# Kernel tuning notes

Measured on AMD Instinct MI355X. Metric: run time of the kernel, lower is better.

The kernel has to match this reference:

```python
import jax, jax.numpy as jnp
import numpy as np
from jax import lax

EMB = 30
K = 5

def leaky(x):
    return jnp.where(x > 0, x, 0.1 * x)

def conv_resid(x, W, b):
    # x: [L, EMB]; W: [EMB, EMB, 3]; SAME trigram conv (matches torch pad=2 + slice) + residual
    y = lax.conv_general_dilated(x.T[None], W, window_strides=(1,), padding=[(1, 1)])  # [1,EMB,L]
    y = leaky(y + b[None, :, None])
    return y[0].T + x

def cosine_sim(A, B):
    num = A @ B.T                                   # [Qa, Qb]
    den = jnp.linalg.norm(A, axis=1)[:, None] * jnp.linalg.norm(B, axis=1)[None, :]
    return num / den

def kmax_pool(sim):
    top = lax.top_k(sim, K)[0]                      # [Q, K] descending
    return jnp.stack([top[:, 0], top.mean(axis=-1)], axis=-1)  # [Q, 2]

def get_output(pools, w, W1, W2):
    temp = jnp.concatenate(pools, axis=-1)          # [Q, 6]
    lo = leaky(temp @ W1.T) @ W2.T                  # [Q, 1]
    lo = lo[:, 0] * w
    return lo.sum() / lo.shape[0]

def setup_inputs() -> dict:
    key = jax.random.key(0)
    ks = jax.random.split(key, 12)
    Q, D = 2048, 8192
    inp = {
        "doc1_embeds": jax.random.normal(ks[0], (D, EMB), jnp.float32),
        "doc2_embeds": jax.random.normal(ks[1], (D, EMB), jnp.float32),
        "question_embeds": jax.random.normal(ks[2], (Q, EMB), jnp.float32),
        "q_idfs": jax.random.uniform(ks[3], (Q, 1), jnp.float32),
        "gaf": jax.random.uniform(ks[4], (4,), jnp.float32),
        "baf": jax.random.uniform(ks[5], (4,), jnp.float32),
        "W_conv": jax.random.normal(ks[6], (EMB, EMB, 3), jnp.float32) * 0.1,
        "b_conv": jax.random.normal(ks[7], (EMB,), jnp.float32) * 0.1,
        "W_qw": jax.random.normal(ks[8], (1, EMB + 1), jnp.float32) * 0.1,
        "W_q1": jax.random.normal(ks[9], (8, 6), jnp.float32) * 0.3,
        "W_q2": jax.random.normal(ks[10], (1, 8), jnp.float32) * 0.3,
        "W_out": jax.random.normal(ks[11], (1, 5), jnp.float32) * 0.3,
    }
    return inp

def reference(doc1_embeds, doc2_embeds, question_embeds, q_idfs, gaf, baf,
              W_conv, b_conv, W_qw, W_q1, W_q2, W_out):
    sim_i_d1 = cosine_sim(question_embeds, doc1_embeds)
    sim_i_d2 = cosine_sim(question_embeds, doc2_embeds)
    sim_oh_d1 = (sim_i_d1 > 1 - 0.001).astype(jnp.float32)
    sim_oh_d2 = (sim_i_d2 > 1 - 0.001).astype(jnp.float32)
    q_conv = conv_resid(question_embeds, W_conv, b_conv)
    d1_conv = conv_resid(doc1_embeds, W_conv, b_conv)
    d2_conv = conv_resid(doc2_embeds, W_conv, b_conv)
    sim_s_d1 = cosine_sim(q_conv, d1_conv)
    sim_s_d2 = cosine_sim(q_conv, d2_conv)
    q_weights = jax.nn.softmax((jnp.concatenate([q_conv, q_idfs], axis=-1) @ W_qw.T)[:, 0])
    doc1_emit = get_output([kmax_pool(sim_oh_d1), kmax_pool(sim_i_d1), kmax_pool(sim_s_d1)], q_weights, W_q1, W_q2)
    doc2_emit = get_output([kmax_pool(sim_oh_d2), kmax_pool(sim_i_d2), kmax_pool(sim_s_d2)], q_weights, W_q1, W_q2)
    good_out = jnp.concatenate([gaf, doc1_emit[None]]) @ W_out.T  # [1]
    bad_out = jnp.concatenate([baf, doc2_emit[None]]) @ W_out.T   # [1]
    loss1 = jnp.sum(jax.nn.relu(1.0 + bad_out - good_out), axis=-1)
    return (loss1, good_out, bad_out)
```

## Files before the change

### kernel.cpp

```cpp
#include <hip/hip_runtime.h>
#include <hip/hip_bf16.h>
#include <math.h>

#define EMB 30
#define NS 64
#define JT 128
#define SUB 64

typedef __attribute__((ext_vector_type(8))) short bf16x8;
typedef __attribute__((ext_vector_type(4))) float f32x4;
typedef __attribute__((ext_vector_type(4))) unsigned u32x4;
typedef __attribute__((ext_vector_type(2))) _Float16 f16x2;

__device__ __forceinline__ float leakyf(float x) { return x > 0.0f ? x : 0.1f * x; }

__device__ __forceinline__ unsigned short f2b(float x) {
  __hip_bfloat16 h = __float2bfloat16(x);
  union { __hip_bfloat16 h; unsigned short u; } cv;
  cv.h = h;
  return cv.u;
}

__device__ __forceinline__ unsigned pkmax(unsigned a, unsigned b) {
  unsigned d;
  asm("v_pk_max_f16 %0, %1, %2" : "=v"(d) : "v"(a), "v"(b));
  return d;
}
__device__ __forceinline__ unsigned pkmin(unsigned a, unsigned b) {
  unsigned d;
  asm("v_pk_min_f16 %0, %1, %2" : "=v"(d) : "v"(a), "v"(b));
  return d;
}
__device__ __forceinline__ unsigned cvtpku(float a, float b) {
  return __builtin_bit_cast(unsigned, __builtin_amdgcn_cvt_pkrtz(a, b));
}

__device__ __forceinline__ void ins5h(unsigned (&t)[5], unsigned v) {
  unsigned n0 = pkmax(t[0], v);
  unsigned n1 = pkmax(pkmin(t[0], v), t[1]);
  unsigned n2 = pkmax(pkmin(t[1], v), t[2]);
  unsigned n3 = pkmax(pkmin(t[2], v), t[3]);
  unsigned n4 = pkmax(pkmin(t[3], v), t[4]);
  t[0] = n0; t[1] = n1; t[2] = n2; t[3] = n3; t[4] = n4;
}

__device__ __forceinline__ void merge5h(unsigned (&a)[5], const unsigned (&b)[5]) {
  unsigned c0 = pkmax(a[0], b[0]);
  unsigned c1 = pkmax(pkmax(pkmin(a[0], b[0]), a[1]), b[1]);
  unsigned c2 = pkmax(pkmax(pkmin(a[0], b[1]), pkmin(a[1], b[0])), pkmax(a[2], b[2]));
  unsigned c3 = pkmax(pkmax(pkmin(a[0], b[2]), pkmin(a[1], b[1])),
                      pkmax(pkmin(a[2], b[0]), pkmax(a[3], b[3])));
  unsigned c4 = pkmax(pkmax(pkmax(pkmin(a[0], b[3]), pkmin(a[1], b[2])),
                            pkmax(pkmin(a[2], b[1]), pkmin(a[3], b[0]))),
                      pkmax(a[4], b[4]));
  a[0] = c0; a[1] = c1; a[2] = c2; a[3] = c3; a[4] = c4;
}

__device__ __forceinline__ void merge5(float (&a)[5], const float (&b)[5]) {
  float c0 = fmaxf(a[0], b[0]);
  float c1 = fmaxf(fmaxf(fminf(a[0], b[0]), a[1]), b[1]);
  float c2 = fmaxf(fmaxf(fminf(a[0], b[1]), fminf(a[1], b[0])), fmaxf(a[2], b[2]));
  float c3 = fmaxf(fmaxf(fminf(a[0], b[2]), fminf(a[1], b[1])),
                   fmaxf(fminf(a[2], b[0]), fmaxf(a[3], b[3])));
  float c4 = fmaxf(fmaxf(fmaxf(fminf(a[0], b[3]), fminf(a[1], b[2])),
                         fmaxf(fminf(a[2], b[1]), fminf(a[3], b[0]))),
                   fmaxf(a[4], b[4]));
  a[0] = c0; a[1] = c1; a[2] = c2; a[3] = c3; a[4] = c4;
}

__global__ __launch_bounds__(256) void prep_all_kernel(
    const float* __restrict__ Xq, const float* __restrict__ X1,
    const float* __restrict__ X2, int Q, int D,
    const float* __restrict__ Wc, const float* __restrict__ bc,
    const float* __restrict__ qidf, const float* __restrict__ Wqw,
    unsigned short* __restrict__ qr, unsigned short* __restrict__ qc,
    unsigned short* __restrict__ cmb, float* __restrict__ logits) {
  __shared__ float sX[66 * EMB];
  __shared__ float sW[EMB * EMB * 3];
  __shared__ float sB[EMB];
  __shared__ float sQw[EMB + 1];
  int tid = threadIdx.x;
  int nbQ = Q >> 6, nbD = D >> 6;
  int b = blockIdx.x;
  const float* X;
  int L, l0, slot = 0;
  bool isQ = false;
  if (b < nbQ) { X = Xq; L = Q; l0 = b << 6; isQ = true; }
  else if (b < nbQ + nbD) { X = X1; L = D; l0 = (b - nbQ) << 6; slot = 0; }
  else { X = X2; L = D; l0 = (b - nbQ - nbD) << 6; slot = 2; }

  for (int idx = tid; idx < EMB * EMB * 3; idx += 256) sW[idx] = Wc[idx];
  if (tid < EMB) sB[tid] = bc[tid];
  if (tid < EMB + 1) sQw[tid] = Wqw[tid];
  int base = l0 * EMB - EMB;
  int lim = L * EMB;
  for (int idx = tid; idx < 66 * EMB; idx += 256) {
    int g = base + idx;
    sX[idx] = (g >= 0 && g < lim) ? X[g] : 0.0f;
  }
  __syncthreads();

  int r = tid >> 2, sub = tid & 3;
  int l = l0 + r;
  int o0 = sub * 8;
  const float* xmP = sX + r * EMB;
  const float* x0P = sX + (r + 1) * EMB;
  const float* xpP = sX + (r + 2) * EMB;
  const float* wP  = sW + o0 * 90;

  float acc[8];
#pragma unroll
  for (int oo = 0; oo < 8; ++oo)
    acc[oo] = (o0 + oo < EMB) ? sB[o0 + oo] : 0.0f;
  float sr = 0.0f;
  for (int i = 0; i < EMB; ++i) {
    float xm = xmP[i], x0v = x0P[i], xp = xpP[i];
    sr += x0v * x0v;
#pragma unroll
    for (int oo = 0; oo < 8; ++oo) {
      if (o0 + oo < EMB) {
        acc[oo] += wP[oo * 90 + i * 3 + 0] * xm;
        acc[oo] += wP[oo * 90 + i * 3 + 1] * x0v;
        acc[oo] += wP[oo * 90 + i * 3 + 2] * xp;
      }
    }
  }
  float y[8];
  float sc = 0.0f, lg = 0.0f;
#pragma unroll
  for (int oo = 0; oo < 8; ++oo) {
    if (o0 + oo < EMB) {
      float v = leakyf(acc[oo]) + x0P[o0 + oo];
      y[oo] = v;
      sc += v * v;
      lg += v * sQw[o0 + oo];
    } else y[oo] = 0.0f;
  }
  sc += __shfl_xor(sc, 1); sc += __shfl_xor(sc, 2);
  lg += __shfl_xor(lg, 1); lg += __shfl_xor(lg, 2);
  float rnr = 1.0f / sqrtf(sr);
  float rnc = 1.0f / sqrtf(sc);
  if (isQ && sub == 0) logits[l] = lg + qidf[l] * sQw[EMB];

  unsigned rd[4], cd[4];
#pragma unroll
  for (int kk = 0; kk < 4; ++kk) {
    int k = sub * 4 + kk;
    if (k < 15) {
      rd[kk] = (unsigned)f2b(x0P[2 * k] * rnr) | ((unsigned)f2b(x0P[2 * k + 1] * rnr) << 16);
      int oo = 2 * k - o0;
      cd[kk] = (unsigned)f2b(y[oo] * rnc) | ((unsigned)f2b(y[oo + 1] * rnc) << 16);
    } else { rd[kk] = 0u; cd[kk] = 0u; }
  }
  if (isQ) {
    unsigned* rw = (unsigned*)(qr + (size_t)l * 32);
    unsigned* cw = (unsigned*)(qc + (size_t)l * 32);
#pragma unroll
    for (int kk = 0; kk < 4; ++kk) { rw[sub * 4 + kk] = rd[kk]; cw[sub * 4 + kk] = cd[kk]; }
  } else {
    unsigned* rowp = (unsigned*)(cmb + (size_t)l * 128);
    int sx = (l & 7) << 2;
#pragma unroll
    for (int kk = 0; kk < 4; ++kk) {
      int k = sub * 4 + kk;
      rowp[(slot * 16 + k) ^ sx]       = rd[kk];
      rowp[((slot + 1) * 16 + k) ^ sx] = cd[kk];
    }
  }
}

__global__ __launch_bounds__(256, 4) void main_kernel(
    const unsigned short* __restrict__ qrA, const unsigned short* __restrict__ qcA,
    const unsigned* __restrict__ cmb32,
    float* __restrict__ partials, int Q, int D) {
  __shared__ __align__(16) unsigned lds[2][SUB * 64];
  int tid = threadIdx.x;
  int wave = tid >> 6, lane = tid & 63;
  int lo = lane & 15, hi = lane >> 4;
  int qt = blockIdx.x >> 6, ds = blockIdx.x & (NS - 1);
  int qb0 = qt * 128 + wave * 32;
  bf16x8 aR0 = *(const bf16x8*)(qrA + (size_t)(qb0 + lo) * 32 + hi * 8);
  bf16x8 aC0 = *(const bf16x8*)(qcA + (size_t)(qb0 + lo) * 32 + hi * 8);
  bf16x8 aR1 = *(const bf16x8*)(qrA + (size_t)(qb0 + 16 + lo) * 32 + hi * 8);
  bf16x8 aC1 = *(const bf16x8*)(qcA + (size_t)(qb0 + 16 + lo) * 32 + hi * 8);

  unsigned t[4][5];
#pragma unroll
  for (int li = 0; li < 4; ++li)
#pragma unroll
    for (int k = 0; k < 5; ++k) t[li][k] = 0xC000C000u;

  const u32x4* gsrc = (const u32x4*)(cmb32 + (size_t)ds * JT * 64);
  u32x4 R[4];
#pragma unroll
  for (int i = 0; i < 4; ++i) R[i] = gsrc[i * 256 + tid];
#pragma unroll
  for (int i = 0; i < 4; ++i) ((u32x4*)lds[0])[i * 256 + tid] = R[i];

  int swzA = ((lo & 7) << 2);
  int c0 = (0  + hi * 4) ^ swzA;
  int c1 = (16 + hi * 4) ^ swzA;
  int c2 = (32 + hi * 4) ^ swzA;
  int c3 = (48 + hi * 4) ^ swzA;

#pragma unroll 1
  for (int st = 0; st < 2; ++st) {
    __syncthreads();
    if (st == 0) {
#pragma unroll
      for (int i = 0; i < 4; ++i) R[i] = gsrc[1024 + i * 256 + tid];
    }
    const unsigned* L = lds[st];
#pragma unroll
    for (int it = 0; it < 4; ++it) {
      const unsigned* rp = L + (it * 16 + lo) * 64;
      bf16x8 X0 = *(const bf16x8*)(rp + c0);
      bf16x8 X1 = *(const bf16x8*)(rp + c1);
      bf16x8 X2 = *(const bf16x8*)(rp + c2);
      bf16x8 X3 = *(const bf16x8*)(rp + c3);
      f32x4 z = {0.0f, 0.0f, 0.0f, 0.0f};
      f32x4 s0a = __builtin_amdgcn_mfma_f32_16x16x32_bf16(X0, aR0, z, 0, 0, 0);
      f32x4 s1a = __builtin_amdgcn_mfma_f32_16x16x32_bf16(X1, aC0, z, 0, 0, 0);
      f32x4 s2a = __builtin_amdgcn_mfma_f32_16x16x32_bf16(X2, aR0, z, 0, 0, 0);
      f32x4 s3a = __builtin_amdgcn_mfma_f32_16x16x32_bf16(X3, aC0, z, 0, 0, 0);
      f32x4 s0b = __builtin_amdgcn_mfma_f32_16x16x32_bf16(X0, aR1, z, 0, 0, 0);
      f32x4 s1b = __builtin_amdgcn_mfma_f32_16x16x32_bf16(X1, aC1, z, 0, 0, 0);
      f32x4 s2b = __builtin_amdgcn_mfma_f32_16x16x32_bf16(X2, aR1, z, 0, 0, 0);
      f32x4 s3b = __builtin_amdgcn_mfma_f32_16x16x32_bf16(X3, aC1, z, 0, 0, 0);
#pragma unroll
      for (int r = 0; r < 4; ++r) {
        ins5h(t[0], cvtpku(s0a[r], s2a[r]));
        ins5h(t[1], cvtpku(s1a[r], s3a[r]));
        ins5h(t[2], cvtpku(s0b[r], s2b[r]));
        ins5h(t[3], cvtpku(s1b[r], s3b[r]));
      }
    }
    __syncthreads();
    if (st == 0) {
#pragma unroll
      for (int i = 0; i < 4; ++i) ((u32x4*)lds[1])[i * 256 + tid] = R[i];
    }
  }

#pragma unroll
  for (int li = 0; li < 4; ++li) {
    unsigned b[5];
#pragma unroll
    for (int k = 0; k < 5; ++k)
      b[k] = (unsigned)__builtin_amdgcn_ds_swizzle((int)t[li][k], 0x401F);
    merge5h(t[li], b);
  }
#pragma unroll
  for (int li = 0; li < 4; ++li) {
    unsigned b[5];
#pragma unroll
    for (int k = 0; k < 5; ++k) b[k] = (unsigned)__shfl_xor((int)t[li][k], 32);
    merge5h(t[li], b);
  }

  if (lane < 16) {
#pragma unroll
    for (int qs = 0; qs < 2; ++qs) {
      int q = qb0 + qs * 16 + lo;
      float* dst = partials + ((size_t)q * NS + ds) * 20;
#pragma unroll
      for (int k = 0; k < 5; ++k) {
        f16x2 t0 = __builtin_bit_cast(f16x2, t[qs * 2 + 0][k]);
        f16x2 t1 = __builtin_bit_cast(f16x2, t[qs * 2 + 1][k]);
        dst[k]      = (float)t0[0];
        dst[5 + k]  = (float)t1[0];
        dst[10 + k] = (float)t0[1];
        dst[15 + k] = (float)t1[1];
      }
    }
  }
}

__global__ __launch_bounds__(256) void pool_kernel(
    const float* __restrict__ logits, const float* __restrict__ partials,
    const float* __restrict__ W1, const float* __restrict__ W2,
    float* __restrict__ blockSums, int Q) {
  __shared__ float sred[4];
  __shared__ float r1[4], r2[4];
  int tid = threadIdx.x;
  int lane = tid & 63, wave = tid >> 6;

  float lmax = -3.0e38f;
  for (int q = tid; q < Q; q += 256) lmax = fmaxf(lmax, logits[q]);
#pragma unroll
  for (int m = 1; m < 64; m <<= 1) lmax = fmaxf(lmax, __shfl_xor(lmax, m));
  if (lane == 0) sred[wave] = lmax;
  __syncthreads();
  float M = fmaxf(fmaxf(sred[0], sred[1]), fmaxf(sred[2], sred[3]));
  __syncthreads();
  float lsum = 0.0f;
  for (int q = tid; q < Q; q += 256) lsum += expf(logits[q] - M);
#pragma unroll
  for (int m = 1; m < 64; m <<= 1) lsum += __shfl_xor(lsum, m);
  if (lane == 0) sred[wave] = lsum;
  __syncthreads();
  float rS = 1.0f / (sred[0] + sred[1] + sred[2] + sred[3]);

  int qglob = blockIdx.x * 4 + wave;
  const float* p0 = partials + ((size_t)qglob * NS + lane) * 20;
  float T[4][5];
#pragma unroll
  for (int li = 0; li < 4; ++li)
#pragma unroll
    for (int k = 0; k < 5; ++k) T[li][k] = p0[li * 5 + k];
#pragma unroll
  for (int m = 32; m >= 1; m >>= 1) {
#pragma unroll
    for (int li = 0; li < 4; ++li) {
      float b[5];
#pragma unroll
      for (int k = 0; k < 5; ++k) b[k] = __shfl_xor(T[li][k], m);
      merge5(T[li], b);
    }
  }
  if (lane == 0) {
    float w = expf(logits[qglob] - M) * rS;
    float s1 = 0.0f, s2 = 0.0f;
#pragma unroll
    for (int d = 0; d < 2; ++d) {
      const float (&Ti)[5] = T[d ? 2 : 0];
      const float (&Ts)[5] = T[d ? 3 : 1];
      float c = 0.0f;
#pragma unroll
      for (int k = 0; k < 5; ++k) c += (Ti[k] > 0.999f) ? 1.0f : 0.0f;
      float tmp[6];
      tmp[0] = (Ti[0] > 0.999f) ? 1.0f : 0.0f;
      tmp[1] = c * 0.2f;
      tmp[2] = Ti[0];
      tmp[3] = (Ti[0] + Ti[1] + Ti[2] + Ti[3] + Ti[4]) * 0.2f;
      tmp[4] = Ts[0];
      tmp[5] = (Ts[0] + Ts[1] + Ts[2] + Ts[3] + Ts[4]) * 0.2f;
      float lov = 0.0f;
#pragma unroll
      for (int r = 0; r < 8; ++r) {
        float h = 0.0f;
#pragma unroll
        for (int cidx = 0; cidx < 6; ++cidx) h += W1[r * 6 + cidx] * tmp[cidx];
        lov += W2[r] * leakyf(h);
      }
      if (d == 0) s1 = lov * w; else s2 = lov * w;
    }
    r1[wave] = s1; r2[wave] = s2;
  }
  __syncthreads();
  if (tid == 0) {
    blockSums[blockIdx.x * 2]     = r1[0] + r1[1] + r1[2] + r1[3];
    blockSums[blockIdx.x * 2 + 1] = r2[0] + r2[1] + r2[2] + r2[3];
  }
}

__global__ __launch_bounds__(64) void final_kernel(
    const float* __restrict__ blockSums, int nBlocks,
    const float* __restrict__ gaf, const float* __restrict__ baf,
    const float* __restrict__ Wout, float* __restrict__ out, int Q) {
  int tid = threadIdx.x;
  float s1 = 0.0f, s2 = 0.0f;
  for (int b = tid; b < nBlocks; b += 64) {
    s1 += blockSums[b * 2];
    s2 += blockSums[b * 2 + 1];
  }
#pragma unroll
  for (int m = 1; m < 64; m <<= 1) { s1 += __shfl_xor(s1, m); s2 += __shfl_xor(s2, m); }
  if (tid == 0) {
    float e1 = s1 / (float)Q, e2 = s2 / (float)Q;
    float good = gaf[0] * Wout[0] + gaf[1] * Wout[1] + gaf[2] * Wout[2] + gaf[3] * Wout[3] + e1 * Wout[4];
    float bad  = baf[0] * Wout[0] + baf[1] * Wout[1] + baf[2] * Wout[2] + baf[3] * Wout[3] + e2 * Wout[4];
    float loss = fmaxf(0.0f, 1.0f + bad - good);
    out[0] = loss; out[1] = good; out[2] = bad;
  }
}

extern "C" void kernel_launch(void* const* d_in, const int* in_sizes, int n_in,
                              void* d_out, int out_size, void* d_ws, size_t ws_size,
                              hipStream_t stream) {
  const float* d1   = (const float*)d_in[0];
  const float* d2   = (const float*)d_in[1];
  const float* qe   = (const float*)d_in[2];
  const float* qidf = (const float*)d_in[3];
  const float* gaf  = (const float*)d_in[4];
  const float* baf  = (const float*)d_in[5];
  const float* Wc   = (const float*)d_in[6];
  const float* bc   = (const float*)d_in[7];
  const float* Wqw  = (const float*)d_in[8];
  const float* Wq1  = (const float*)d_in[9];
  const float* Wq2  = (const float*)d_in[10];
  const float* Wout = (const float*)d_in[11];
  int D = in_sizes[0] / EMB;
  int Q = in_sizes[2] / EMB;

  unsigned short* us = (unsigned short*)d_ws;
  unsigned short* cmb = us; us += (size_t)D * 128;
  unsigned short* qrA = us; us += (size_t)Q * 32;
  unsigned short* qcA = us; us += (size_t)Q * 32;
  float* fp = (float*)us;
  float* logits    = fp; fp += Q;
  float* partials  = fp; fp += (size_t)Q * NS * 20;
  float* blockSums = fp; fp += (Q / 4) * 2;

  int grid = (Q >> 6) + 2 * (D >> 6);
  prep_all_kernel<<<grid, 256, 0, stream>>>(qe, d1, d2, Q, D, Wc, bc, qidf, Wqw,
                                            qrA, qcA, cmb, logits);
  main_kernel<<<(Q / 128) * NS, 256, 0, stream>>>(qrA, qcA, (const unsigned*)cmb,
                                                  partials, Q, D);
  pool_kernel<<<Q / 4, 256, 0, stream>>>(logits, partials, Wq1, Wq2, blockSums, Q);
  final_kernel<<<1, 64, 0, stream>>>(blockSums, Q / 4, gaf, baf, Wout, (float*)d_out, Q);
}
```

Baseline: 55.10 us.

## Software-pipeline MFMA loop, vectorize partial stores, fold final reduction into pool kernel

Issues the global tile load before the query fragment loads. Software-pipelines the LDS-load / MFMA / top-5 insert sequence so MFMAs for one sub-tile overlap the insertion work of the previous one. Writes the 20 partial floats per query as five 16-byte vector stores instead of scalar stores. Removes the separate final kernel by having the last pool block, found through an atomic counter, do the final reduction, at the cost of an extra memset launch and a threadfence.

```diff
diff --git a/kernel.cpp b/kernel.cpp
--- a/kernel.cpp
+++ b/kernel.cpp
@@ -179,6 +179,12 @@
   int lo = lane & 15, hi = lane >> 4;
   int qt = blockIdx.x >> 6, ds = blockIdx.x & (NS - 1);
   int qb0 = qt * 128 + wave * 32;
+
+  const u32x4* gsrc = (const u32x4*)(cmb32 + (size_t)ds * JT * 64);
+  u32x4 R[4];
+#pragma unroll
+  for (int i = 0; i < 4; ++i) R[i] = gsrc[i * 256 + tid];
+
   bf16x8 aR0 = *(const bf16x8*)(qrA + (size_t)(qb0 + lo) * 32 + hi * 8);
   bf16x8 aC0 = *(const bf16x8*)(qcA + (size_t)(qb0 + lo) * 32 + hi * 8);
   bf16x8 aR1 = *(const bf16x8*)(qrA + (size_t)(qb0 + 16 + lo) * 32 + hi * 8);
@@ -190,10 +196,6 @@
 #pragma unroll
     for (int k = 0; k < 5; ++k) t[li][k] = 0xC000C000u;
 
-  const u32x4* gsrc = (const u32x4*)(cmb32 + (size_t)ds * JT * 64);
-  u32x4 R[4];
-#pragma unroll
-  for (int i = 0; i < 4; ++i) R[i] = gsrc[i * 256 + tid];
 #pragma unroll
   for (int i = 0; i < 4; ++i) ((u32x4*)lds[0])[i * 256 + tid] = R[i];
 
@@ -203,6 +205,30 @@
   int c2 = (32 + hi * 4) ^ swzA;
   int c3 = (48 + hi * 4) ^ swzA;
 
+  f32x4 s0a, s1a, s2a, s3a, s0b, s1b, s2b, s3b;
+
+#define LOADX(IT, X0, X1, X2, X3) {                                            \
+    const unsigned* rp = L + ((IT) * 16 + lo) * 64;                            \
+    X0 = *(const bf16x8*)(rp + c0); X1 = *(const bf16x8*)(rp + c1);            \
+    X2 = *(const bf16x8*)(rp + c2); X3 = *(const bf16x8*)(rp + c3); }
+
+#define MFMA8(X0, X1, X2, X3) {                                                \
+    f32x4 z = {0.0f, 0.0f, 0.0f, 0.0f};                                        \
+    s0a = __builtin_amdgcn_mfma_f32_16x16x32_bf16(X0, aR0, z, 0, 0, 0);        \
+    s1a = __builtin_amdgcn_mfma_f32_16x16x32_bf16(X1, aC0, z, 0, 0, 0);        \
+    s2a = __builtin_amdgcn_mfma_f32_16x16x32_bf16(X2, aR0, z, 0, 0, 0);        \
+    s3a = __builtin_amdgcn_mfma_f32_16x16x32_bf16(X3, aC0, z, 0, 0, 0);        \
+    s0b = __builtin_amdgcn_mfma_f32_16x16x32_bf16(X0, aR1, z, 0, 0, 0);        \
+    s1b = __builtin_amdgcn_mfma_f32_16x16x32_bf16(X1, aC1, z, 0, 0, 0);        \
+    s2b = __builtin_amdgcn_mfma_f32_16x16x32_bf16(X2, aR1, z, 0, 0, 0);        \
+    s3b = __builtin_amdgcn_mfma_f32_16x16x32_bf16(X3, aC1, z, 0, 0, 0); }
+
+#define CONSUME() _Pragma("unroll") for (int r = 0; r < 4; ++r) {              \
+    ins5h(t[0], cvtpku(s0a[r], s2a[r]));                                       \
+    ins5h(t[1], cvtpku(s1a[r], s3a[r]));                                       \
+    ins5h(t[2], cvtpku(s0b[r], s2b[r]));                                       \
+    ins5h(t[3], cvtpku(s1b[r], s3b[r])); }
+
 #pragma unroll 1
   for (int st = 0; st < 2; ++st) {
     __syncthreads();
@@ -211,36 +237,28 @@
       for (int i = 0; i < 4; ++i) R[i] = gsrc[1024 + i * 256 + tid];
     }
     const unsigned* L = lds[st];
-#pragma unroll
-    for (int it = 0; it < 4; ++it) {
-      const unsigned* rp = L + (it * 16 + lo) * 64;
-      bf16x8 X0 = *(const bf16x8*)(rp + c0);
-      bf16x8 X1 = *(const bf16x8*)(rp + c1);
-      bf16x8 X2 = *(const bf16x8*)(rp + c2);
-      bf16x8 X3 = *(const bf16x8*)(rp + c3);
-      f32x4 z = {0.0f, 0.0f, 0.0f, 0.0f};
-      f32x4 s0a = __builtin_amdgcn_mfma_f32_16x16x32_bf16(X0, aR0, z, 0, 0, 0);
-      f32x4 s1a = __builtin_amdgcn_mfma_f32_16x16x32_bf16(X1, aC0, z, 0, 0, 0);
-      f32x4 s2a = __builtin_amdgcn_mfma_f32_16x16x32_bf16(X2, aR0, z, 0, 0, 0);
-      f32x4 s3a = __builtin_amdgcn_mfma_f32_16x16x32_bf16(X3, aC0, z, 0, 0, 0);
-      f32x4 s0b = __builtin_amdgcn_mfma_f32_16x16x32_bf16(X0, aR1, z, 0, 0, 0);
-      f32x4 s1b = __builtin_amdgcn_mfma_f32_16x16x32_bf16(X1, aC1, z, 0, 0, 0);
-      f32x4 s2b = __builtin_amdgcn_mfma_f32_16x16x32_bf16(X2, aR1, z, 0, 0, 0);
-      f32x4 s3b = __builtin_amdgcn_mfma_f32_16x16x32_bf16(X3, aC1, z, 0, 0, 0);
-#pragma unroll
-      for (int r = 0; r < 4; ++r) {
-        ins5h(t[0], cvtpku(s0a[r], s2a[r]));
-        ins5h(t[1], cvtpku(s1a[r], s3a[r]));
-        ins5h(t[2], cvtpku(s0b[r], s2b[r]));
-        ins5h(t[3], cvtpku(s1b[r], s3b[r]));
-      }
-    }
+    bf16x8 Xa0, Xa1, Xa2, Xa3, Xb0, Xb1, Xb2, Xb3;
+    LOADX(0, Xa0, Xa1, Xa2, Xa3)
+    MFMA8(Xa0, Xa1, Xa2, Xa3)
+    LOADX(1, Xb0, Xb1, Xb2, Xb3)
+    CONSUME()
+    MFMA8(Xb0, Xb1, Xb2, Xb3)
+    LOADX(2, Xa0, Xa1, Xa2, Xa3)
+    CONSUME()
+    MFMA8(Xa0, Xa1, Xa2, Xa3)
+    LOADX(3, Xb0, Xb1, Xb2, Xb3)
+    CONSUME()
+    MFMA8(Xb0, Xb1, Xb2, Xb3)
+    CONSUME()
     __syncthreads();
     if (st == 0) {
 #pragma unroll
       for (int i = 0; i < 4; ++i) ((u32x4*)lds[1])[i * 256 + tid] = R[i];
     }
   }
+#undef LOADX
+#undef MFMA8
+#undef CONSUME
 
 #pragma unroll
   for (int li = 0; li < 4; ++li) {
@@ -263,15 +281,19 @@
     for (int qs = 0; qs < 2; ++qs) {
       int q = qb0 + qs * 16 + lo;
       float* dst = partials + ((size_t)q * NS + ds) * 20;
+      float a[20];
 #pragma unroll
       for (int k = 0; k < 5; ++k) {
         f16x2 t0 = __builtin_bit_cast(f16x2, t[qs * 2 + 0][k]);
         f16x2 t1 = __builtin_bit_cast(f16x2, t[qs * 2 + 1][k]);
-        dst[k]      = (float)t0[0];
-        dst[5 + k]  = (float)t1[0];
-        dst[10 + k] = (float)t0[1];
-        dst[15 + k] = (float)t1[1];
+        a[k]      = (float)t0[0];
+        a[5 + k]  = (float)t1[0];
+        a[10 + k] = (float)t0[1];
+        a[15 + k] = (float)t1[1];
       }
+#pragma unroll
+      for (int v = 0; v < 5; ++v)
+        ((f32x4*)dst)[v] = *(f32x4*)(a + v * 4);
     }
   }
 }
@@ -279,9 +301,12 @@
 __global__ __launch_bounds__(256) void pool_kernel(
     const float* __restrict__ logits, const float* __restrict__ partials,
     const float* __restrict__ W1, const float* __restrict__ W2,
-    float* __restrict__ blockSums, int Q) {
+    const float* __restrict__ gaf, const float* __restrict__ baf,
+    const float* __restrict__ Wout, float* __restrict__ blockSums,
+    int* __restrict__ counter, float* __restrict__ out, int Q) {
   __shared__ float sred[4];
   __shared__ float r1[4], r2[4];
+  __shared__ int isLast;
   int tid = threadIdx.x;
   int lane = tid & 63, wave = tid >> 6;
 
@@ -351,27 +376,29 @@
   if (tid == 0) {
     blockSums[blockIdx.x * 2]     = r1[0] + r1[1] + r1[2] + r1[3];
     blockSums[blockIdx.x * 2 + 1] = r2[0] + r2[1] + r2[2] + r2[3];
-  }
-}
-
-__global__ __launch_bounds__(64) void final_kernel(
-    const float* __restrict__ blockSums, int nBlocks,
-    const float* __restrict__ gaf, const float* __restrict__ baf,
-    const float* __restrict__ Wout, float* __restrict__ out, int Q) {
-  int tid = threadIdx.x;
-  float s1 = 0.0f, s2 = 0.0f;
-  for (int b = tid; b < nBlocks; b += 64) {
-    s1 += blockSums[b * 2];
-    s2 += blockSums[b * 2 + 1];
-  }
-#pragma unroll
-  for (int m = 1; m < 64; m <<= 1) { s1 += __shfl_xor(s1, m); s2 += __shfl_xor(s2, m); }
-  if (tid == 0) {
-    float e1 = s1 / (float)Q, e2 = s2 / (float)Q;
-    float good = gaf[0] * Wout[0] + gaf[1] * Wout[1] + gaf[2] * Wout[2] + gaf[3] * Wout[3] + e1 * Wout[4];
-    float bad  = baf[0] * Wout[0] + baf[1] * Wout[1] + baf[2] * Wout[2] + baf[3] * Wout[3] + e2 * Wout[4];
-    float loss = fmaxf(0.0f, 1.0f + bad - good);
-    out[0] = loss; out[1] = good; out[2] = bad;
+    __threadfence();
+    isLast = (atomicAdd(counter, 1) == (int)gridDim.x - 1) ? 1 : 0;
+  }
+  __syncthreads();
+  if (isLast) {
+    float s1 = 0.0f, s2 = 0.0f;
+    for (int b = tid; b < (int)gridDim.x; b += 256) {
+      s1 += blockSums[b * 2];
+      s2 += blockSums[b * 2 + 1];
+    }
+#pragma unroll
+    for (int m = 1; m < 64; m <<= 1) { s1 += __shfl_xor(s1, m); s2 += __shfl_xor(s2, m); }
+    if (lane == 0) { sred[wave] = s1; r1[wave] = s2; }
+    __syncthreads();
+    if (tid == 0) {
+      float S1 = sred[0] + sred[1] + sred[2] + sred[3];
+      float S2 = r1[0] + r1[1] + r1[2] + r1[3];
+      float e1 = S1 / (float)Q, e2 = S2 / (float)Q;
+      float good = gaf[0] * Wout[0] + gaf[1] * Wout[1] + gaf[2] * Wout[2] + gaf[3] * Wout[3] + e1 * Wout[4];
+      float bad  = baf[0] * Wout[0] + baf[1] * Wout[1] + baf[2] * Wout[2] + baf[3] * Wout[3] + e2 * Wout[4];
+      float loss = fmaxf(0.0f, 1.0f + bad - good);
+      out[0] = loss; out[1] = good; out[2] = bad;
+    }
   }
 }
 
@@ -401,12 +428,16 @@
   float* logits    = fp; fp += Q;
   float* partials  = fp; fp += (size_t)Q * NS * 20;
   float* blockSums = fp; fp += (Q / 4) * 2;
+  int* counter     = (int*)fp; fp += 1;
+
+  hipMemsetAsync(counter, 0, sizeof(int), stream);
 
   int grid = (Q >> 6) + 2 * (D >> 6);
   prep_all_kernel<<<grid, 256, 0, stream>>>(qe, d1, d2, Q, D, Wc, bc, qidf, Wqw,
                                             qrA, qcA, cmb, logits);
   main_kernel<<<(Q / 128) * NS, 256, 0, stream>>>(qrA, qcA, (const unsigned*)cmb,
                                                   partials, Q, D);
-  pool_kernel<<<Q / 4, 256, 0, stream>>>(logits, partials, Wq1, Wq2, blockSums, Q);
-  final_kernel<<<1, 64, 0, stream>>>(blockSums, Q / 4, gaf, baf, Wout, (float*)d_out, Q);
-}
+  pool_kernel<<<Q / 4, 256, 0, stream>>>(logits, partials, Wq1, Wq2,
+                                         gaf, baf, Wout, blockSums, counter,
+                                         (float*)d_out, Q);
+}
```

New measurement: 64.07 us. 16.3% more time.
